# Kernel optimization log

Measured on AMD Instinct MI355X. Metric: run time of the kernel, lower is better.

The kernel has to match this reference:

```python
import jax, jax.numpy as jnp
import numpy as np

B, TE, TD, HE, HD = 4, 512, 256, 128, 256

def setup_inputs() -> dict:
    key = jax.random.key(0)
    k1, k2, k3, k4, k5 = jax.random.split(key, 5)
    return {
        "encoder_out_seq": jax.random.normal(k1, (B, TE, HE), dtype=jnp.float32),
        "decoder_out_seq": jax.random.normal(k2, (B, TD, HD), dtype=jnp.float32),
        "W_a": jax.random.normal(k3, (HE, HE), dtype=jnp.float32) * 0.05,
        "U_a": jax.random.normal(k4, (HD, HE), dtype=jnp.float32) * 0.05,
        "V_a": jax.random.normal(k5, (HE, 1), dtype=jnp.float32) * 0.05,
    }

def reference(encoder_out_seq, decoder_out_seq, W_a, U_a, V_a):
    # Bahdanau additive attention, fully parallel over decoder steps
    # (the original K.rnn scan has no true recurrence: each step is independent).
    Ws = jnp.einsum('bse,ef->bsf', encoder_out_seq, W_a)   # [B,Te,He]
    Uh = jnp.einsum('btd,df->btf', decoder_out_seq, U_a)   # [B,Td,He]
    # [B,Td,Te,He] additive score features
    feat = jnp.tanh(Ws[:, None, :, :] + Uh[:, :, None, :])
    e = jnp.einsum('btsf,f->bts', feat, V_a[:, 0])         # [B,Td,Te]
    e = jax.nn.softmax(e, axis=-1)                         # attention weights
    c = jnp.einsum('bts,bse->bte', e, encoder_out_seq)     # [B,Td,He] contexts
    return (c, e)
```

## Files before the change

### kernel.cpp

```cpp
#include <hip/hip_runtime.h>

#define Bn  4
#define TEn 512
#define TDn 256
#define HEn 128
#define HDn 256

#define KSCALE 2.8853900817779268f

#if __has_builtin(__builtin_amdgcn_exp2f)
#define EXP2(x) __builtin_amdgcn_exp2f(x)
#else
#define EXP2(x) __expf(0.6931471805599453f * (x))
#endif

__device__ __forceinline__ float sigEP(float E, float P) {
    return __builtin_amdgcn_rcpf(fmaf(E, P, 1.0f));
}

__global__ __launch_bounds__(512) void proj_kernel(
    const float* __restrict__ enc, const float* __restrict__ dec,
    const float* __restrict__ W, const float* __restrict__ U,
    float* __restrict__ Ew, float* __restrict__ P)
{
    const int tid = threadIdx.x;
    if (blockIdx.x < 512) {
        __shared__ __align__(16) float enc_lds[4 * HEn];
        const int c  = tid & (HEn - 1);
        const int rl = tid >> 7;
        const int r0 = blockIdx.x * 4;
        enc_lds[tid] = enc[r0 * HEn + tid];
        __syncthreads();
        const float* wc = W + c;
        const float* er = enc_lds + rl * HEn;
        float acc = 0.f;
        #pragma unroll 4
        for (int k = 0; k < HEn; k += 8) {
            float4 e0 = *(const float4*)(er + k);
            float4 e1 = *(const float4*)(er + k + 4);
            acc = fmaf(e0.x, wc[(k + 0) * HEn], acc);
            acc = fmaf(e0.y, wc[(k + 1) * HEn], acc);
            acc = fmaf(e0.z, wc[(k + 2) * HEn], acc);
            acc = fmaf(e0.w, wc[(k + 3) * HEn], acc);
            acc = fmaf(e1.x, wc[(k + 4) * HEn], acc);
            acc = fmaf(e1.y, wc[(k + 5) * HEn], acc);
            acc = fmaf(e1.z, wc[(k + 6) * HEn], acc);
            acc = fmaf(e1.w, wc[(k + 7) * HEn], acc);
        }
        Ew[(r0 + rl) * HEn + c] = EXP2(acc * KSCALE);
    } else {
        __shared__ __align__(16) float dec_lds[4 * HDn];
        __shared__ __align__(16) float part[4][512];
        const int bt0 = (blockIdx.x - 512) * 4;
        dec_lds[tid]       = dec[bt0 * HDn + tid];
        dec_lds[tid + 512] = dec[bt0 * HDn + tid + 512];
        __syncthreads();
        const int f = tid & 127;
        const int p = tid >> 7;
        const float* u = U + (p * 64) * HEn + f;
        float a0 = 0.f, a1 = 0.f, a2 = 0.f, a3 = 0.f;
        #pragma unroll 8
        for (int k = 0; k < 64; ++k) {
            const float uk = u[k * HEn];
            const int kk = p * 64 + k;
            a0 = fmaf(dec_lds[kk],            uk, a0);
            a1 = fmaf(dec_lds[HDn + kk],      uk, a1);
            a2 = fmaf(dec_lds[2 * HDn + kk],  uk, a2);
            a3 = fmaf(dec_lds[3 * HDn + kk],  uk, a3);
        }
        part[p][f]       = a0;
        part[p][128 + f] = a1;
        part[p][256 + f] = a2;
        part[p][384 + f] = a3;
        __syncthreads();
        const int r = tid >> 7;
        const float s = part[0][r * 128 + f] + part[1][r * 128 + f]
                      + part[2][r * 128 + f] + part[3][r * 128 + f];
        P[(bt0 + r) * HEn + f] = EXP2(s * KSCALE);
    }
}

__global__ __launch_bounds__(1024, 4) void attn_kernel(
    const float* __restrict__ enc, const float* __restrict__ V,
    const float* __restrict__ Ew, const float* __restrict__ P,
    float* __restrict__ c_out, float* __restrict__ e_out)
{
    const int b    = blockIdx.x >> 6;
    const int t0   = (blockIdx.x & 63) * 4;
    const int bt0  = b * TDn + t0;
    const int tid  = threadIdx.x;
    const int lane = tid & 63;
    const int wave = tid >> 6;

    __shared__ __align__(16) float sc[4][TEn];
    __shared__ __align__(16) float part[32][512];
    __shared__ float redm[4][8];
    __shared__ float reds[4][8];

    {
        const int s_sub = lane & 7;
        const int f0    = (lane >> 3) * 16;
        float4 vn[4], uu[4][4];
        float sv = 0.f;
        #pragma unroll
        for (int j = 0; j < 4; ++j) {
            float4 v = *(const float4*)(V + f0 + 4 * j);
            sv += v.x + v.y + v.z + v.w;
            vn[j] = make_float4(-2.f * v.x, -2.f * v.y, -2.f * v.z, -2.f * v.w);
            #pragma unroll
            for (int r = 0; r < 4; ++r)
                uu[r][j] = *(const float4*)(P + (bt0 + r) * HEn + f0 + 4 * j);
        }
        const float* wsb = Ew + (b * TEn + wave * 32) * HEn;
        #pragma unroll
        for (int ci = 0; ci < 4; ++ci) {
            const float* wp = wsb + (ci * 8 + s_sub) * HEn + f0;
            float x0 = sv, x1 = sv, x2 = sv, x3 = sv;
            #pragma unroll
            for (int j = 0; j < 4; ++j) {
                float4 w = ((const float4*)wp)[j];
                x0 = fmaf(vn[j].x, sigEP(w.x, uu[0][j].x), x0);
                x1 = fmaf(vn[j].x, sigEP(w.x, uu[1][j].x), x1);
                x2 = fmaf(vn[j].x, sigEP(w.x, uu[2][j].x), x2);
                x3 = fmaf(vn[j].x, sigEP(w.x, uu[3][j].x), x3);
                x0 = fmaf(vn[j].y, sigEP(w.y, uu[0][j].y), x0);
                x1 = fmaf(vn[j].y, sigEP(w.y, uu[1][j].y), x1);
                x2 = fmaf(vn[j].y, sigEP(w.y, uu[2][j].y), x2);
                x3 = fmaf(vn[j].y, sigEP(w.y, uu[3][j].y), x3);
                x0 = fmaf(vn[j].z, sigEP(w.z, uu[0][j].z), x0);
                x1 = fmaf(vn[j].z, sigEP(w.z, uu[1][j].z), x1);
                x2 = fmaf(vn[j].z, sigEP(w.z, uu[2][j].z), x2);
                x3 = fmaf(vn[j].z, sigEP(w.z, uu[3][j].z), x3);
                x0 = fmaf(vn[j].w, sigEP(w.w, uu[0][j].w), x0);
                x1 = fmaf(vn[j].w, sigEP(w.w, uu[1][j].w), x1);
                x2 = fmaf(vn[j].w, sigEP(w.w, uu[2][j].w), x2);
                x3 = fmaf(vn[j].w, sigEP(w.w, uu[3][j].w), x3);
            }
            x0 += __shfl_xor(x0, 8, 64);  x1 += __shfl_xor(x1, 8, 64);
            x2 += __shfl_xor(x2, 8, 64);  x3 += __shfl_xor(x3, 8, 64);
            x0 += __shfl_xor(x0, 16, 64); x1 += __shfl_xor(x1, 16, 64);
            x2 += __shfl_xor(x2, 16, 64); x3 += __shfl_xor(x3, 16, 64);
            x0 += __shfl_xor(x0, 32, 64); x1 += __shfl_xor(x1, 32, 64);
            x2 += __shfl_xor(x2, 32, 64); x3 += __shfl_xor(x3, 32, 64);
            if (lane < 8) {
                const int s = wave * 32 + ci * 8 + lane;
                sc[0][s] = x0; sc[1][s] = x1; sc[2][s] = x2; sc[3][s] = x3;
            }
        }
    }
    __syncthreads();

    {
        const int s  = tid & 511;
        const int r0 = (tid >> 9) * 2;
        const int w8 = wave & 7;
        const float v0 = sc[r0][s];
        const float v1 = sc[r0 + 1][s];
        float m0 = v0, m1 = v1;
        #pragma unroll
        for (int off = 32; off; off >>= 1) {
            m0 = fmaxf(m0, __shfl_xor(m0, off, 64));
            m1 = fmaxf(m1, __shfl_xor(m1, off, 64));
        }
        if (lane == 0) { redm[r0][w8] = m0; redm[r0 + 1][w8] = m1; }
        __syncthreads();
        float bm0 = redm[r0][0], bm1 = redm[r0 + 1][0];
        #pragma unroll
        for (int w = 1; w < 8; ++w) {
            bm0 = fmaxf(bm0, redm[r0][w]);
            bm1 = fmaxf(bm1, redm[r0 + 1][w]);
        }
        const float ex0 = __expf(v0 - bm0);
        const float ex1 = __expf(v1 - bm1);
        float s0 = ex0, s1 = ex1;
        #pragma unroll
        for (int off = 32; off; off >>= 1) {
            s0 += __shfl_xor(s0, off, 64);
            s1 += __shfl_xor(s1, off, 64);
        }
        if (lane == 0) { reds[r0][w8] = s0; reds[r0 + 1][w8] = s1; }
        __syncthreads();
        float bs0 = reds[r0][0], bs1 = reds[r0 + 1][0];
        #pragma unroll
        for (int w = 1; w < 8; ++w) { bs0 += reds[r0][w]; bs1 += reds[r0 + 1][w]; }
        const float e0 = ex0 * __builtin_amdgcn_rcpf(bs0);
        const float e1 = ex1 * __builtin_amdgcn_rcpf(bs1);
        e_out[(bt0 + r0) * TEn + s]     = e0;
        e_out[(bt0 + r0 + 1) * TEn + s] = e1;
        sc[r0][s]     = e0;
        sc[r0 + 1][s] = e1;
    }
    __syncthreads();

    {
        const int hl = tid & 31;
        const int sp = tid >> 5;
        const float* eb = enc + (b * TEn + sp * 16) * HEn + hl * 4;
        float4 a0 = {0,0,0,0}, a1 = {0,0,0,0}, a2 = {0,0,0,0}, a3 = {0,0,0,0};
        #pragma unroll 4
        for (int i = 0; i < 16; ++i) {
            const int s = sp * 16 + i;
            const float4 ev = *(const float4*)(eb + i * HEn);
            const float w0 = sc[0][s], w1 = sc[1][s];
            const float w2 = sc[2][s], w3 = sc[3][s];
            a0.x = fmaf(w0, ev.x, a0.x); a1.x = fmaf(w1, ev.x, a1.x);
            a2.x = fmaf(w2, ev.x, a2.x); a3.x = fmaf(w3, ev.x, a3.x);
            a0.y = fmaf(w0, ev.y, a0.y); a1.y = fmaf(w1, ev.y, a1.y);
            a2.y = fmaf(w2, ev.y, a2.y); a3.y = fmaf(w3, ev.y, a3.y);
            a0.z = fmaf(w0, ev.z, a0.z); a1.z = fmaf(w1, ev.z, a1.z);
            a2.z = fmaf(w2, ev.z, a2.z); a3.z = fmaf(w3, ev.z, a3.z);
            a0.w = fmaf(w0, ev.w, a0.w); a1.w = fmaf(w1, ev.w, a1.w);
            a2.w = fmaf(w2, ev.w, a2.w); a3.w = fmaf(w3, ev.w, a3.w);
        }
        *(float4*)&part[sp][0   + hl * 4] = a0;
        *(float4*)&part[sp][128 + hl * 4] = a1;
        *(float4*)&part[sp][256 + hl * 4] = a2;
        *(float4*)&part[sp][384 + hl * 4] = a3;
    }
    __syncthreads();
    if (tid < 512) {
        const int r = tid >> 7, h = tid & 127;
        float s0 = 0.f, s1 = 0.f;
        #pragma unroll
        for (int p = 0; p < 32; p += 2) {
            s0 += part[p][r * 128 + h];
            s1 += part[p + 1][r * 128 + h];
        }
        c_out[(bt0 + r) * HEn + h] = s0 + s1;
    }
}

extern "C" void kernel_launch(void* const* d_in, const int* in_sizes, int n_in,
                              void* d_out, int out_size, void* d_ws, size_t ws_size,
                              hipStream_t stream) {
    const float* enc = (const float*)d_in[0];
    const float* dec = (const float*)d_in[1];
    const float* W   = (const float*)d_in[2];
    const float* U   = (const float*)d_in[3];
    const float* V   = (const float*)d_in[4];
    float* out   = (float*)d_out;
    float* c_out = out;
    float* e_out = out + Bn * TDn * HEn;
    float* Ew    = (float*)d_ws;
    float* P     = Ew + Bn * TEn * HEn;

    proj_kernel<<<768, 512, 0, stream>>>(enc, dec, W, U, Ew, P);
    attn_kernel<<<(Bn * TDn) / 4, 1024, 0, stream>>>(enc, V, Ew, P, c_out, e_out);
}
```

Measured before the change: 86.02 us.

## Fuse projection and attention kernels into one cooperative kernel with grid sync

Merges the projection kernel and the attention kernel into a single cooperative launch. Each block computes 8 rows of exp-scaled encoder projections to global memory and its own 4 decoder projections into LDS, then waits on a grid-wide barrier before the attention phase. This removes the second launch and the global round trip for the decoder projection. In exchange it adds the cost of a grid barrier and requires all 256 blocks of 1024 threads to be co-resident.

```diff
diff --git a/kernel.cpp b/kernel.cpp
--- a/kernel.cpp
+++ b/kernel.cpp
@@ -1,4 +1,7 @@
 #include <hip/hip_runtime.h>
+#include <hip/hip_cooperative_groups.h>
+
+namespace cg = cooperative_groups;
 
 #define Bn  4
 #define TEn 512
@@ -18,19 +21,35 @@
     return __builtin_amdgcn_rcpf(fmaf(E, P, 1.0f));
 }
 
-__global__ __launch_bounds__(512) void proj_kernel(
+__global__ __launch_bounds__(1024, 4) void fused_kernel(
     const float* __restrict__ enc, const float* __restrict__ dec,
     const float* __restrict__ W, const float* __restrict__ U,
-    float* __restrict__ Ew, float* __restrict__ P)
+    const float* __restrict__ V, float* __restrict__ Ew,
+    float* __restrict__ c_out, float* __restrict__ e_out)
 {
-    const int tid = threadIdx.x;
-    if (blockIdx.x < 512) {
-        __shared__ __align__(16) float enc_lds[4 * HEn];
-        const int c  = tid & (HEn - 1);
+    const int b    = blockIdx.x >> 6;
+    const int t0   = (blockIdx.x & 63) * 4;
+    const int bt0  = b * TDn + t0;
+    const int tid  = threadIdx.x;
+    const int lane = tid & 63;
+    const int wave = tid >> 6;
+
+    __shared__ __align__(16) float enc_lds[8 * HEn];
+    __shared__ __align__(16) float dec_lds[4 * HDn];
+    __shared__ __align__(16) float p_lds[4][HEn];
+    __shared__ __align__(16) float sc[4][TEn];
+    __shared__ __align__(16) float part[32][512];
+    __shared__ float redm[4][8];
+    __shared__ float reds[4][8];
+
+    const int er0 = blockIdx.x * 8;
+    enc_lds[tid] = enc[er0 * HEn + tid];
+    dec_lds[tid] = dec[bt0 * HDn + tid];
+    __syncthreads();
+
+    {
+        const int c  = tid & 127;
         const int rl = tid >> 7;
-        const int r0 = blockIdx.x * 4;
-        enc_lds[tid] = enc[r0 * HEn + tid];
-        __syncthreads();
         const float* wc = W + c;
         const float* er = enc_lds + rl * HEn;
         float acc = 0.f;
@@ -47,22 +66,18 @@
             acc = fmaf(e1.z, wc[(k + 6) * HEn], acc);
             acc = fmaf(e1.w, wc[(k + 7) * HEn], acc);
         }
-        Ew[(r0 + rl) * HEn + c] = EXP2(acc * KSCALE);
-    } else {
-        __shared__ __align__(16) float dec_lds[4 * HDn];
-        __shared__ __align__(16) float part[4][512];
-        const int bt0 = (blockIdx.x - 512) * 4;
-        dec_lds[tid]       = dec[bt0 * HDn + tid];
-        dec_lds[tid + 512] = dec[bt0 * HDn + tid + 512];
-        __syncthreads();
+        Ew[(er0 + rl) * HEn + c] = EXP2(acc * KSCALE);
+    }
+
+    {
         const int f = tid & 127;
         const int p = tid >> 7;
-        const float* u = U + (p * 64) * HEn + f;
+        const float* u = U + (p * 32) * HEn + f;
         float a0 = 0.f, a1 = 0.f, a2 = 0.f, a3 = 0.f;
         #pragma unroll 8
-        for (int k = 0; k < 64; ++k) {
+        for (int k = 0; k < 32; ++k) {
             const float uk = u[k * HEn];
-            const int kk = p * 64 + k;
+            const int kk = p * 32 + k;
             a0 = fmaf(dec_lds[kk],            uk, a0);
             a1 = fmaf(dec_lds[HDn + kk],      uk, a1);
             a2 = fmaf(dec_lds[2 * HDn + kk],  uk, a2);
@@ -72,30 +87,20 @@
         part[p][128 + f] = a1;
         part[p][256 + f] = a2;
         part[p][384 + f] = a3;
-        __syncthreads();
-        const int r = tid >> 7;
-        const float s = part[0][r * 128 + f] + part[1][r * 128 + f]
-                      + part[2][r * 128 + f] + part[3][r * 128 + f];
-        P[(bt0 + r) * HEn + f] = EXP2(s * KSCALE);
-    }
-}
-
-__global__ __launch_bounds__(1024, 4) void attn_kernel(
-    const float* __restrict__ enc, const float* __restrict__ V,
-    const float* __restrict__ Ew, const float* __restrict__ P,
-    float* __restrict__ c_out, float* __restrict__ e_out)
-{
-    const int b    = blockIdx.x >> 6;
-    const int t0   = (blockIdx.x & 63) * 4;
-    const int bt0  = b * TDn + t0;
-    const int tid  = threadIdx.x;
-    const int lane = tid & 63;
-    const int wave = tid >> 6;
-
-    __shared__ __align__(16) float sc[4][TEn];
-    __shared__ __align__(16) float part[32][512];
-    __shared__ float redm[4][8];
-    __shared__ float reds[4][8];
+    }
+    __syncthreads();
+    if (tid < 512) {
+        const int r = tid >> 7, f = tid & 127;
+        float s0 = 0.f, s1 = 0.f;
+        #pragma unroll
+        for (int p = 0; p < 8; p += 2) {
+            s0 += part[p][r * 128 + f];
+            s1 += part[p + 1][r * 128 + f];
+        }
+        p_lds[r][f] = EXP2((s0 + s1) * KSCALE);
+    }
+
+    cg::this_grid().sync();
 
     {
         const int s_sub = lane & 7;
@@ -109,7 +114,7 @@
             vn[j] = make_float4(-2.f * v.x, -2.f * v.y, -2.f * v.z, -2.f * v.w);
             #pragma unroll
             for (int r = 0; r < 4; ++r)
-                uu[r][j] = *(const float4*)(P + (bt0 + r) * HEn + f0 + 4 * j);
+                uu[r][j] = *(const float4*)(&p_lds[r][f0 + 4 * j]);
         }
         const float* wsb = Ew + (b * TEn + wave * 32) * HEn;
         #pragma unroll
@@ -242,8 +247,9 @@
     float* c_out = out;
     float* e_out = out + Bn * TDn * HEn;
     float* Ew    = (float*)d_ws;
-    float* P     = Ew + Bn * TEn * HEn;
-
-    proj_kernel<<<768, 512, 0, stream>>>(enc, dec, W, U, Ew, P);
-    attn_kernel<<<(Bn * TDn) / 4, 1024, 0, stream>>>(enc, V, Ew, P, c_out, e_out);
+
+    void* args[] = { (void*)&enc, (void*)&dec, (void*)&W, (void*)&U,
+                     (void*)&V, (void*)&Ew, (void*)&c_out, (void*)&e_out };
+    hipLaunchCooperativeKernel((const void*)fused_kernel,
+                               dim3(Bn * TDn / 4), dim3(1024), args, 0, stream);
 }
```

Result: slower. 122.4 us (+42.2%).
